# Optimization experiments

Hardware: AMD Instinct MI355X
Metric: run time of the kernel (lower is better)

Reference implementation:

```python
import jax, jax.numpy as jnp
import numpy as np

N = 65536
E = 524288
G = 8192
HID = 512


def setup_inputs() -> dict:
    key = jax.random.key(0)
    ks = jax.random.split(key, 10)
    v_x_raw = jax.random.normal(ks[0], (N, 3), dtype=jnp.float32)
    H_decoded = jax.random.normal(ks[1], (N, HID), dtype=jnp.float32)
    x_t = 2.0 * jax.random.normal(ks[2], (N, 3), dtype=jnp.float32)
    row = jax.random.randint(ks[3], (E,), 0, N)
    # avoid self edges (fully_connect_edges excludes i==j)
    col = (row + 1 + jax.random.randint(ks[4], (E,), 0, N - 1)) % N
    edges = jnp.stack([row, col]).astype(jnp.int64)
    gen_idx = (jnp.arange(G, dtype=jnp.int32) * (N // G)).astype(jnp.int32)
    gen_mask = jnp.zeros((N,), dtype=bool).at[gen_idx].set(True)
    W_proj = jax.random.normal(ks[5], (HID, HID // 2), dtype=jnp.float32) / np.sqrt(HID)
    b_proj = jnp.zeros((HID // 2,), dtype=jnp.float32)
    w_bond = jax.random.normal(ks[6], (HID // 2, 1), dtype=jnp.float32) / np.sqrt(HID // 2)
    b_bond = jnp.zeros((1,), dtype=jnp.float32)
    w_val = jax.random.normal(ks[7], (HID // 2, 1), dtype=jnp.float32) / np.sqrt(HID // 2)
    b_val = jnp.zeros((1,), dtype=jnp.float32)
    return {"v_x_raw": v_x_raw, "H_decoded": H_decoded, "x_t": x_t, "edges": edges,
            "gen_mask": gen_mask, "gen_idx": gen_idx, "W_proj": W_proj, "b_proj": b_proj,
            "w_bond": w_bond, "b_bond": b_bond, "w_val": w_val, "b_val": b_val}


def _constrained_velocity(v_x_raw, H_decoded, x_t, edges, gen_mask, gen_idx,
                          W_proj, b_proj, w_bond, b_bond, w_val, b_val):
    TARGET_LEN = 1.5   # target bond length
    MIN_DIST = 1.0     # clash cutoff
    EPS = 1e-8

    feat = H_decoded @ W_proj + b_proj                      # [N, HID//2]

    # --- bond length corrections: vectorized scatter-add over edges ---
    row, col = edges[0], edges[1]
    diff = x_t[row] - x_t[col]                              # [E, 3]
    dist = jnp.sqrt(jnp.maximum(jnp.sum(diff * diff, -1), 1e-24)) + EPS  # [E]
    edge_gate = (gen_mask[row] | gen_mask[col]).astype(x_t.dtype)
    # force_magnitude * force_direction = (d - L)/d * diff/d
    force = ((dist - TARGET_LEN) / (dist * dist) * edge_gate)[:, None] * diff  # [E,3]
    bond_corr = jnp.zeros_like(x_t).at[row].add(force).at[col].add(-force)

    # --- clash corrections: dense pairwise over generated atoms ---
    xg = x_t[gen_idx]                                       # [G, 3]
    sq = jnp.sum(xg * xg, -1)                               # [G]
    d2 = sq[:, None] + sq[None, :] - 2.0 * (xg @ xg.T)      # [G, G]
    d = jnp.sqrt(jnp.maximum(d2, 1e-24)) + EPS
    pair_mask = (d < MIN_DIST) & ~jnp.eye(xg.shape[0], dtype=bool)
    # (min - d)/d * (x_i - x_j)/d  ->  coef_ij * (x_i - x_j)
    coef = jnp.where(pair_mask, (MIN_DIST - d) / (d * d), 0.0)  # [G, G]
    corr_g = xg * jnp.sum(coef, 1, keepdims=True) - coef @ xg   # [G, 3]
    clash_corr = jnp.zeros_like(x_t).at[gen_idx].add(corr_g)

    bond_w = jax.nn.sigmoid(feat @ w_bond + b_bond)         # [N, 1]
    clash_w = jax.nn.sigmoid(feat @ w_val + b_val)          # [N, 1]
    return v_x_raw - 0.1 * bond_w * bond_corr - 0.05 * clash_w * clash_corr


def reference(v_x_raw, H_decoded, x_t, edges, gen_mask, gen_idx,
              W_proj, b_proj, w_bond, b_bond, w_val, b_val):
    return _constrained_velocity(v_x_raw, H_decoded, x_t, edges, gen_mask, gen_idx,
                                 W_proj, b_proj, w_bond, b_bond, w_val, b_val)
```

## Files before the change

kernel.cpp:

```cpp
#include <hip/hip_runtime.h>
#include <math.h>

#define HID_DIM  512
#define HIDH_DIM 256
#define ZBLOCKS  125
#define JC       256

__global__ __launch_bounds__(256) void prep_kernel(
        const unsigned int* __restrict__ ew,
        const float* __restrict__ Wp,  const float* __restrict__ bp,
        const float* __restrict__ wb,  const float* __restrict__ bb,
        const float* __restrict__ wv,  const float* __restrict__ bv,
        const int* __restrict__ gen_idx, const float* __restrict__ x_t,
        float4* __restrict__ zbase, int zcount,
        float* __restrict__ u_bond, float* __restrict__ u_val,
        float* __restrict__ cvals, int* __restrict__ flag,
        float* __restrict__ xgx, float* __restrict__ xgy, float* __restrict__ xgz,
        unsigned char* __restrict__ mask, int* __restrict__ gpos,
        int n, int G, int GB) {
    int b = blockIdx.x, t = threadIdx.x;
    if (b < ZBLOCKS) {
        const float4 z = make_float4(0.f, 0.f, 0.f, 0.f);
        for (int i = b * 256 + t; i < zcount; i += ZBLOCKS * 256) zbase[i] = z;
    } else if (b == ZBLOCKS) {
        if (t < 64) {
            unsigned int v = ew[2 * t + 1];
            unsigned long long bl = __ballot(v == 0u);
            if (t == 0) flag[0] = (bl == 0xFFFFFFFFFFFFFFFFULL) ? 1 : 0;
        }
        __shared__ float s1[256], s2[256];
        float p1 = (t < HIDH_DIM) ? bp[t] * wb[t] : 0.f;
        float p2 = (t < HIDH_DIM) ? bp[t] * wv[t] : 0.f;
        s1[t] = p1; s2[t] = p2;
        __syncthreads();
        for (int s = 128; s > 0; s >>= 1) {
            if (t < s) { s1[t] += s1[t + s]; s2[t] += s2[t + s]; }
            __syncthreads();
        }
        if (t == 0) { cvals[0] = s1[0] + bb[0]; cvals[1] = s2[0] + bv[0]; }
    } else if (b <= ZBLOCKS + 2) {
        int k = (b - ZBLOCKS - 1) * 256 + t;
        if (k < HID_DIM) {
            const float* wrow = Wp + (size_t)k * HIDH_DIM;
            float ub = 0.f, uv = 0.f;
            for (int m = 0; m < HIDH_DIM; ++m) {
                float w = wrow[m];
                ub += w * wb[m];
                uv += w * wv[m];
            }
            u_bond[k] = ub;
            u_val[k]  = uv;
        }
    } else if (b < ZBLOCKS + 3 + GB) {
        int g = (b - ZBLOCKS - 3) * 256 + t;
        if (g < G) {
            int idx = gen_idx[g];
            xgx[g] = x_t[3 * idx + 0];
            xgy[g] = x_t[3 * idx + 1];
            xgz[g] = x_t[3 * idx + 2];
        }
    } else {
        int base = ((b - ZBLOCKS - 3 - GB) * 256 + t) * 8;
        for (int k = 0; k < 8; ++k) {
            int i = base + k;
            if (i >= n) break;
            int lo = 0, hi = G - 1, g = -1;
            while (lo <= hi) {
                int mid = (lo + hi) >> 1;
                int v = gen_idx[mid];
                if (v == i) { g = mid; break; }
                if (v < i) lo = mid + 1; else hi = mid - 1;
            }
            mask[i] = (g >= 0) ? 1 : 0;
            if (g >= 0) gpos[i] = g;
        }
    }
}

__device__ __forceinline__ float wave_reduce_sum(float v) {
    #pragma unroll
    for (int off = 32; off > 0; off >>= 1) v += __shfl_down(v, off, 64);
    return v;
}

__global__ __launch_bounds__(256) void mega_kernel(
        const float* __restrict__ H,
        const float* __restrict__ u_bond, const float* __restrict__ u_val,
        const float* __restrict__ cvals,
        const unsigned int* __restrict__ ew, const int* __restrict__ flag_p,
        const float* __restrict__ x_t, const unsigned char* __restrict__ mask,
        const float* __restrict__ xgx, const float* __restrict__ xgy,
        const float* __restrict__ xgz,
        float* __restrict__ bond_corr,
        float* __restrict__ gsum, float* __restrict__ gvec,
        float* __restrict__ bond_w, float* __restrict__ clash_w,
        int n, int E, int G, int NBC, int NBB, int CXB) {
    __shared__ __align__(16) float sx[JC];
    __shared__ __align__(16) float sy[JC];
    __shared__ __align__(16) float sz[JC];
    int b = blockIdx.x, t = threadIdx.x;

    if (b < NBC) {
        int i = (b & (CXB - 1)) * 256 + t;
        int j = (b / CXB) * JC + t;
        sx[t] = (j < G) ? xgx[j] : 1e30f;
        sy[t] = (j < G) ? xgy[j] : 1e30f;
        sz[t] = (j < G) ? xgz[j] : 1e30f;
        __syncthreads();
        if (i >= G) return;
        float xi = xgx[i], yi = xgy[i], zi = xgz[i];
        float csum = 0.f, cx = 0.f, cy = 0.f, cz = 0.f;
#define PROC(XS, YS, ZS) do {                                           \
            float dx = xi - (XS), dy = yi - (YS), dz = zi - (ZS);       \
            float d2 = fmaf(dx, dx, fmaf(dy, dy, dz * dz));             \
            float rm = __builtin_amdgcn_rsqf(d2);                       \
            float coef = fmaxf(fmaf(rm, rm, -rm), 0.0f);                \
            csum += coef;                                               \
            cx = fmaf(coef, (XS), cx);                                  \
            cy = fmaf(coef, (YS), cy);                                  \
            cz = fmaf(coef, (ZS), cz);                                  \
        } while (0)
        #pragma unroll 4
        for (int tt = 0; tt < JC; tt += 4) {
            float4 ax = *reinterpret_cast<const float4*>(&sx[tt]);
            float4 ay = *reinterpret_cast<const float4*>(&sy[tt]);
            float4 az = *reinterpret_cast<const float4*>(&sz[tt]);
            PROC(ax.x, ay.x, az.x);
            PROC(ax.y, ay.y, az.y);
            PROC(ax.z, ay.z, az.z);
            PROC(ax.w, ay.w, az.w);
        }
#undef PROC
        atomicAdd(&gsum[i], csum);
        atomicAdd(&gvec[3 * i + 0], cx);
        atomicAdd(&gvec[3 * i + 1], cy);
        atomicAdd(&gvec[3 * i + 2], cz);
    } else if (b < NBC + NBB) {
        int e = (b - NBC) * 256 + t;
        if (e >= E) return;
        int f = flag_p[0];
        int row, col;
        if (f) {
            row = (int)ew[2 * (size_t)e];
            col = (int)ew[2 * ((size_t)E + e)];
        } else {
            row = (int)ew[e];
            col = (int)ew[(size_t)E + e];
        }
        if ((unsigned)row >= (unsigned)n || (unsigned)col >= (unsigned)n) return;
        if (!(mask[row] | mask[col])) return;
        float dx = x_t[3 * row + 0] - x_t[3 * col + 0];
        float dy = x_t[3 * row + 1] - x_t[3 * col + 1];
        float dz = x_t[3 * row + 2] - x_t[3 * col + 2];
        float d2 = dx * dx + dy * dy + dz * dz;
        float dist = sqrtf(fmaxf(d2, 1e-24f)) + 1e-8f;
        float s = (dist - 1.5f) / (dist * dist);
        float fx = s * dx, fy = s * dy, fz = s * dz;
        atomicAdd(&bond_corr[3 * row + 0],  fx);
        atomicAdd(&bond_corr[3 * row + 1],  fy);
        atomicAdd(&bond_corr[3 * row + 2],  fz);
        atomicAdd(&bond_corr[3 * col + 0], -fx);
        atomicAdd(&bond_corr[3 * col + 1], -fy);
        atomicAdd(&bond_corr[3 * col + 2], -fz);
    } else {
        int gid = (b - NBC - NBB) * 256 + t;
        int wave = gid >> 6;
        int lane = t & 63;
        if (wave >= n) return;
        const float* h = H + (size_t)wave * HID_DIM;
        float sb = 0.f, sv = 0.f;
        #pragma unroll
        for (int c = 0; c < 2; ++c) {
            int o = c * 256 + lane * 4;
            float4 hv = *reinterpret_cast<const float4*>(h + o);
            float4 ub = *reinterpret_cast<const float4*>(u_bond + o);
            float4 uv = *reinterpret_cast<const float4*>(u_val + o);
            sb += hv.x * ub.x + hv.y * ub.y + hv.z * ub.z + hv.w * ub.w;
            sv += hv.x * uv.x + hv.y * uv.y + hv.z * uv.z + hv.w * uv.w;
        }
        sb = wave_reduce_sum(sb);
        sv = wave_reduce_sum(sv);
        if (lane == 0) {
            float zb = sb + cvals[0];
            float zv = sv + cvals[1];
            bond_w[wave]  = 1.f / (1.f + expf(-zb));
            clash_w[wave] = 1.f / (1.f + expf(-zv));
        }
    }
}

__global__ void final_kernel(const float* __restrict__ v_x,
                             const float* __restrict__ bond_w,
                             const float* __restrict__ clash_w,
                             const float* __restrict__ bond_corr,
                             const unsigned char* __restrict__ mask,
                             const int* __restrict__ gpos,
                             const float* __restrict__ xgx,
                             const float* __restrict__ xgy,
                             const float* __restrict__ xgz,
                             const float* __restrict__ gsum,
                             const float* __restrict__ gvec,
                             float* __restrict__ out, int n) {
    int i = blockIdx.x * blockDim.x + threadIdx.x;
    if (i >= n) return;
    float bw = 0.1f * bond_w[i];
    float ox = v_x[3 * i + 0] - bw * bond_corr[3 * i + 0];
    float oy = v_x[3 * i + 1] - bw * bond_corr[3 * i + 1];
    float oz = v_x[3 * i + 2] - bw * bond_corr[3 * i + 2];
    if (mask[i]) {
        int g = gpos[i];
        float s  = gsum[g];
        float cw = 0.05f * clash_w[i];
        ox -= cw * (xgx[g] * s - gvec[3 * g + 0]);
        oy -= cw * (xgy[g] * s - gvec[3 * g + 1]);
        oz -= cw * (xgz[g] * s - gvec[3 * g + 2]);
    }
    out[3 * i + 0] = ox;
    out[3 * i + 1] = oy;
    out[3 * i + 2] = oz;
}

extern "C" void kernel_launch(void* const* d_in, const int* in_sizes, int n_in,
                              void* d_out, int out_size, void* d_ws, size_t ws_size,
                              hipStream_t stream) {
    const float* v_x_raw = (const float*)d_in[0];
    const float* H       = (const float*)d_in[1];
    const float* x_t     = (const float*)d_in[2];
    const unsigned int* edges_w = (const unsigned int*)d_in[3];
    const int* gen_idx   = (const int*)d_in[5];
    const float* W_proj  = (const float*)d_in[6];
    const float* b_proj  = (const float*)d_in[7];
    const float* w_bond  = (const float*)d_in[8];
    const float* b_bond  = (const float*)d_in[9];
    const float* w_val   = (const float*)d_in[10];
    const float* b_val   = (const float*)d_in[11];

    const int n = in_sizes[0] / 3;
    const int E = in_sizes[3] / 2;
    const int G = in_sizes[5];
    const int GB = (G + 255) / 256;

    char* ws = (char*)d_ws;
    float* bond_corr  = (float*)(ws);
    float* gsum       = (float*)(ws + (size_t)n * 12);
    float* gvec       = (float*)(ws + (size_t)n * 12 + (size_t)G * 4);
    size_t zbytes = (size_t)n * 12 + (size_t)G * 16;
    size_t off = (zbytes + 15) & ~(size_t)15;
    int zcount = (int)(off / 16);
    unsigned char* mask = (unsigned char*)(ws + off); off += ((size_t)n + 15) & ~(size_t)15;
    int*   gpos    = (int*)(ws + off);                off += (size_t)n * 4;
    float* bond_w  = (float*)(ws + off);              off += (size_t)n * 4;
    float* clash_w = (float*)(ws + off);              off += (size_t)n * 4;
    float* u_bond  = (float*)(ws + off);              off += HID_DIM * 4;
    float* u_val   = (float*)(ws + off);              off += HID_DIM * 4;
    float* cvals   = (float*)(ws + off);              off += 16;
    int*   flag    = (int*)(ws + off);                off += 16;
    float* xgx     = (float*)(ws + off);              off += (size_t)G * 4;
    float* xgy     = (float*)(ws + off);              off += (size_t)G * 4;
    float* xgz     = (float*)(ws + off);              off += (size_t)G * 4;

    const int MB  = (n + 2047) / 2048;
    const int CXB = GB;
    const int NBC = CXB * ((G + JC - 1) / JC);
    const int NBB = (E + 255) / 256;
    const int NBG = (n * 64 + 255) / 256;

    prep_kernel<<<ZBLOCKS + 3 + GB + MB, 256, 0, stream>>>(
        edges_w, W_proj, b_proj, w_bond, b_bond, w_val, b_val,
        gen_idx, x_t, (float4*)ws, zcount,
        u_bond, u_val, cvals, flag, xgx, xgy, xgz, mask, gpos, n, G, GB);

    mega_kernel<<<NBC + NBB + NBG, 256, 0, stream>>>(
        H, u_bond, u_val, cvals, edges_w, flag, x_t, mask,
        xgx, xgy, xgz, bond_corr, gsum, gvec, bond_w, clash_w,
        n, E, G, NBC, NBB, CXB);

    final_kernel<<<(n + 255) / 256, 256, 0, stream>>>(
        v_x_raw, bond_w, clash_w, bond_corr, mask, gpos,
        xgx, xgy, xgz, gsum, gvec, (float*)d_out, n);
}
```

Baseline: 100.00 us.

## Replace clash atomics with partial buffers, batch GEMV rows per wave, reorder blocks

```diff
diff --git a/kernel.cpp b/kernel.cpp
--- a/kernel.cpp
+++ b/kernel.cpp
@@ -83,6 +83,10 @@
     return v;
 }
 
+__device__ __forceinline__ float dot4(float4 a, float4 b) {
+    return a.x * b.x + a.y * b.y + a.z * b.z + a.w * b.w;
+}
+
 __global__ __launch_bounds__(256) void mega_kernel(
         const float* __restrict__ H,
         const float* __restrict__ u_bond, const float* __restrict__ u_val,
@@ -92,17 +96,18 @@
         const float* __restrict__ xgx, const float* __restrict__ xgy,
         const float* __restrict__ xgz,
         float* __restrict__ bond_corr,
-        float* __restrict__ gsum, float* __restrict__ gvec,
+        float* __restrict__ gsum_p, float* __restrict__ gvec_p,
         float* __restrict__ bond_w, float* __restrict__ clash_w,
-        int n, int E, int G, int NBC, int NBB, int CXB) {
+        int n, int E, int G, int NBC, int NBG, int CXB) {
     __shared__ __align__(16) float sx[JC];
     __shared__ __align__(16) float sy[JC];
     __shared__ __align__(16) float sz[JC];
     int b = blockIdx.x, t = threadIdx.x;
 
     if (b < NBC) {
-        int i = (b & (CXB - 1)) * 256 + t;
-        int j = (b / CXB) * JC + t;
+        int yc = b / CXB;
+        int i  = (b - yc * CXB) * 256 + t;
+        int j  = yc * JC + t;
         sx[t] = (j < G) ? xgx[j] : 1e30f;
         sy[t] = (j < G) ? xgy[j] : 1e30f;
         sz[t] = (j < G) ? xgz[j] : 1e30f;
@@ -131,12 +136,55 @@
             PROC(ax.w, ay.w, az.w);
         }
 #undef PROC
-        atomicAdd(&gsum[i], csum);
-        atomicAdd(&gvec[3 * i + 0], cx);
-        atomicAdd(&gvec[3 * i + 1], cy);
-        atomicAdd(&gvec[3 * i + 2], cz);
-    } else if (b < NBC + NBB) {
-        int e = (b - NBC) * 256 + t;
+        size_t p = (size_t)yc * G + i;
+        gsum_p[p] = csum;
+        gvec_p[3 * p + 0] = cx;
+        gvec_p[3 * p + 1] = cy;
+        gvec_p[3 * p + 2] = cz;
+    } else if (b < NBC + NBG) {
+        int bb = b - NBC;
+        int w = t >> 6, lane = t & 63;
+        int row0 = bb * 32 + w * 8;
+        int o0 = lane * 4, o1 = 256 + lane * 4;
+        float4 ub0 = *reinterpret_cast<const float4*>(u_bond + o0);
+        float4 ub1 = *reinterpret_cast<const float4*>(u_bond + o1);
+        float4 uv0 = *reinterpret_cast<const float4*>(u_val + o0);
+        float4 uv1 = *reinterpret_cast<const float4*>(u_val + o1);
+        float c0 = cvals[0], c1 = cvals[1];
+        #pragma unroll
+        for (int r = 0; r < 8; r += 2) {
+            int ra = row0 + r, rb = ra + 1;
+            bool va = (ra < n), vb = (rb < n);
+            const float* ha = H + (size_t)(va ? ra : 0) * HID_DIM;
+            const float* hb = H + (size_t)(vb ? rb : 0) * HID_DIM;
+            float4 a0 = *reinterpret_cast<const float4*>(ha + o0);
+            float4 a1 = *reinterpret_cast<const float4*>(ha + o1);
+            float4 b0 = *reinterpret_cast<const float4*>(hb + o0);
+            float4 b1 = *reinterpret_cast<const float4*>(hb + o1);
+            float sba = dot4(a0, ub0) + dot4(a1, ub1);
+            float sva = dot4(a0, uv0) + dot4(a1, uv1);
+            float sbb = dot4(b0, ub0) + dot4(b1, ub1);
+            float svb = dot4(b0, uv0) + dot4(b1, uv1);
+            #pragma unroll
+            for (int off = 32; off > 0; off >>= 1) {
+                sba += __shfl_down(sba, off, 64);
+                sva += __shfl_down(sva, off, 64);
+                sbb += __shfl_down(sbb, off, 64);
+                svb += __shfl_down(svb, off, 64);
+            }
+            if (lane == 0) {
+                if (va) {
+                    bond_w[ra]  = 1.f / (1.f + expf(-(sba + c0)));
+                    clash_w[ra] = 1.f / (1.f + expf(-(sva + c1)));
+                }
+                if (vb) {
+                    bond_w[rb]  = 1.f / (1.f + expf(-(sbb + c0)));
+                    clash_w[rb] = 1.f / (1.f + expf(-(svb + c1)));
+                }
+            }
+        }
+    } else {
+        int e = (b - NBC - NBG) * 256 + t;
         if (e >= E) return;
         int f = flag_p[0];
         int row, col;
@@ -162,30 +210,6 @@
         atomicAdd(&bond_corr[3 * col + 0], -fx);
         atomicAdd(&bond_corr[3 * col + 1], -fy);
         atomicAdd(&bond_corr[3 * col + 2], -fz);
-    } else {
-        int gid = (b - NBC - NBB) * 256 + t;
-        int wave = gid >> 6;
-        int lane = t & 63;
-        if (wave >= n) return;
-        const float* h = H + (size_t)wave * HID_DIM;
-        float sb = 0.f, sv = 0.f;
-        #pragma unroll
-        for (int c = 0; c < 2; ++c) {
-            int o = c * 256 + lane * 4;
-            float4 hv = *reinterpret_cast<const float4*>(h + o);
-            float4 ub = *reinterpret_cast<const float4*>(u_bond + o);
-            float4 uv = *reinterpret_cast<const float4*>(u_val + o);
-            sb += hv.x * ub.x + hv.y * ub.y + hv.z * ub.z + hv.w * ub.w;
-            sv += hv.x * uv.x + hv.y * uv.y + hv.z * uv.z + hv.w * uv.w;
-        }
-        sb = wave_reduce_sum(sb);
-        sv = wave_reduce_sum(sv);
-        if (lane == 0) {
-            float zb = sb + cvals[0];
-            float zv = sv + cvals[1];
-            bond_w[wave]  = 1.f / (1.f + expf(-zb));
-            clash_w[wave] = 1.f / (1.f + expf(-zv));
-        }
     }
 }
 
@@ -198,9 +222,9 @@
                              const float* __restrict__ xgx,
                              const float* __restrict__ xgy,
                              const float* __restrict__ xgz,
-                             const float* __restrict__ gsum,
-                             const float* __restrict__ gvec,
-                             float* __restrict__ out, int n) {
+                             const float* __restrict__ gsum_p,
+                             const float* __restrict__ gvec_p,
+                             float* __restrict__ out, int n, int G, int NYC) {
     int i = blockIdx.x * blockDim.x + threadIdx.x;
     if (i >= n) return;
     float bw = 0.1f * bond_w[i];
@@ -209,11 +233,18 @@
     float oz = v_x[3 * i + 2] - bw * bond_corr[3 * i + 2];
     if (mask[i]) {
         int g = gpos[i];
-        float s  = gsum[g];
+        float s = 0.f, vx = 0.f, vy = 0.f, vz = 0.f;
+        for (int yc = 0; yc < NYC; ++yc) {
+            size_t p = (size_t)yc * G + g;
+            s  += gsum_p[p];
+            vx += gvec_p[3 * p + 0];
+            vy += gvec_p[3 * p + 1];
+            vz += gvec_p[3 * p + 2];
+        }
         float cw = 0.05f * clash_w[i];
-        ox -= cw * (xgx[g] * s - gvec[3 * g + 0]);
-        oy -= cw * (xgy[g] * s - gvec[3 * g + 1]);
-        oz -= cw * (xgz[g] * s - gvec[3 * g + 2]);
+        ox -= cw * (xgx[g] * s - vx);
+        oy -= cw * (xgy[g] * s - vy);
+        oz -= cw * (xgz[g] * s - vz);
     }
     out[3 * i + 0] = ox;
     out[3 * i + 1] = oy;
@@ -238,13 +269,12 @@
     const int n = in_sizes[0] / 3;
     const int E = in_sizes[3] / 2;
     const int G = in_sizes[5];
-    const int GB = (G + 255) / 256;
+    const int GB  = (G + 255) / 256;
+    const int NYC = (G + JC - 1) / JC;
 
     char* ws = (char*)d_ws;
-    float* bond_corr  = (float*)(ws);
-    float* gsum       = (float*)(ws + (size_t)n * 12);
-    float* gvec       = (float*)(ws + (size_t)n * 12 + (size_t)G * 4);
-    size_t zbytes = (size_t)n * 12 + (size_t)G * 16;
+    float* bond_corr = (float*)(ws);
+    size_t zbytes = (size_t)n * 12;
     size_t off = (zbytes + 15) & ~(size_t)15;
     int zcount = (int)(off / 16);
     unsigned char* mask = (unsigned char*)(ws + off); off += ((size_t)n + 15) & ~(size_t)15;
@@ -258,24 +288,26 @@
     float* xgx     = (float*)(ws + off);              off += (size_t)G * 4;
     float* xgy     = (float*)(ws + off);              off += (size_t)G * 4;
     float* xgz     = (float*)(ws + off);              off += (size_t)G * 4;
+    float* gsum_p  = (float*)(ws + off);              off += (size_t)NYC * G * 4;
+    float* gvec_p  = (float*)(ws + off);              off += (size_t)NYC * G * 12;
 
     const int MB  = (n + 2047) / 2048;
     const int CXB = GB;
-    const int NBC = CXB * ((G + JC - 1) / JC);
+    const int NBC = CXB * NYC;
+    const int NBG = (n + 31) / 32;
     const int NBB = (E + 255) / 256;
-    const int NBG = (n * 64 + 255) / 256;
 
     prep_kernel<<<ZBLOCKS + 3 + GB + MB, 256, 0, stream>>>(
         edges_w, W_proj, b_proj, w_bond, b_bond, w_val, b_val,
         gen_idx, x_t, (float4*)ws, zcount,
         u_bond, u_val, cvals, flag, xgx, xgy, xgz, mask, gpos, n, G, GB);
 
-    mega_kernel<<<NBC + NBB + NBG, 256, 0, stream>>>(
+    mega_kernel<<<NBC + NBG + NBB, 256, 0, stream>>>(
         H, u_bond, u_val, cvals, edges_w, flag, x_t, mask,
-        xgx, xgy, xgz, bond_corr, gsum, gvec, bond_w, clash_w,
-        n, E, G, NBC, NBB, CXB);
+        xgx, xgy, xgz, bond_corr, gsum_p, gvec_p, bond_w, clash_w,
+        n, E, G, NBC, NBG, CXB);
 
     final_kernel<<<(n + 255) / 256, 256, 0, stream>>>(
         v_x_raw, bond_w, clash_w, bond_corr, mask, gpos,
-        xgx, xgy, xgz, gsum, gvec, (float*)d_out, n);
-}
+        xgx, xgy, xgz, gsum_p, gvec_p, (float*)d_out, n, G, NYC);
+}
```

New measurement: 109.5 us. +9.5%, slower.
